# Kernel optimization log

Hardware: AMD Instinct MI355X
Metric: run time of the kernel (lower is better)

## Reference

```python
import jax, jax.numpy as jnp
import numpy as np

E, R, D, B = 1_000_000, 1_000, 64, 32_768
MARGIN = 1.0


def setup_inputs() -> dict:
    key = jax.random.key(0)
    ks = jax.random.split(key, 8)
    return {
        "ent_embeddings": jax.random.normal(ks[0], (E, D), dtype=jnp.float32) * (1.0 / np.sqrt(D)),
        "rel_matrices": jax.random.normal(ks[1], (R, D * D), dtype=jnp.float32) * (1.0 / D),
        "ph": jax.random.randint(ks[2], (B,), 0, E, dtype=jnp.int32),
        "pt": jax.random.randint(ks[3], (B,), 0, E, dtype=jnp.int32),
        "pr": jax.random.randint(ks[4], (B,), 0, R, dtype=jnp.int32),
        "nh": jax.random.randint(ks[5], (B,), 0, E, dtype=jnp.int32),
        "nt": jax.random.randint(ks[6], (B,), 0, E, dtype=jnp.int32),
        "nr": jax.random.randint(ks[7], (B,), 0, R, dtype=jnp.int32),
    }


def _score(ent, rel, h_idx, t_idx, r_idx):
    # gather: h,t -> [B,D]; r -> [B,D,D]
    h = ent[h_idx]
    t = ent[t_idx]
    r = rel[r_idx].reshape(-1, D, D)
    rt = jnp.einsum('bij,bj->bi', r, t)      # matmul(pr, pt): [B,D]
    # mean over D (keep_dims=False) then sum keepdims -> [B,1]
    return jnp.mean(h * rt, axis=1, keepdims=True)


def reference(ent_embeddings, rel_matrices, ph, pt, pr, nh, nt, nr):
    sp = _score(ent_embeddings, rel_matrices, ph, pt, pr)  # [B,1]
    sn = _score(ent_embeddings, rel_matrices, nh, nt, nr)  # [B,1]
    return jnp.sum(jnp.maximum(0.0, sn - sp + MARGIN))
```

## Files before the change

### kernel.cpp

```cpp
#include <hip/hip_runtime.h>


#define DIM 64
#define BATCH 32768
#define NREL 1000
#define NTASK (2 * BATCH)
#define BINCAP 128
#define RS 68
#define TS 36
#define SENT 0x7F800001u


__global__ __launch_bounds__(256) void scatter_kernel(
    const int* __restrict__ ph, const int* __restrict__ pt,
    const int* __restrict__ pr, const int* __restrict__ nh,
    const int* __restrict__ nt, const int* __restrict__ nr,
    int* __restrict__ cursors, int4* __restrict__ bins,
    unsigned int* __restrict__ pairs, float* __restrict__ out)
{
    int t = blockIdx.x * 256 + threadIdx.x;
    int b = t & (BATCH - 1);
    int side = t >> 15;
    int r  = side ? nr[b] : pr[b];
    int ti = side ? nt[b] : pt[b];
    int hi = side ? nh[b] : ph[b];
    int c = atomicAdd(&cursors[r], 1);
    if (c < BINCAP) bins[r * BINCAP + c] = make_int4(t, ti, hi, 0);
    pairs[b] = SENT;
    if (t == 0) *out = 0.f;
}

__global__ __launch_bounds__(256) void score_kernel(
    const float* __restrict__ ent, const float* __restrict__ rel,
    const int* __restrict__ cursors, const int4* __restrict__ bins,
    unsigned int* __restrict__ pairs, float* __restrict__ out)
{
    const int r = blockIdx.x;
    const int w = threadIdx.x >> 6;
    const int lane = threadIdx.x & 63;

    __shared__ float RT[DIM * RS];
    __shared__ float TT[4 * DIM * TS];
    float* bsum = &RT[64];
    if (threadIdx.x == 0) *bsum = 0.f;

    const float4* rg = (const float4*)(rel + (size_t)r * (DIM * DIM));
    #pragma unroll
    for (int it = 0; it < 4; ++it) {
        int f = threadIdx.x + 256 * it;
        int i = f >> 4, jc = f & 15;
        float4 v = rg[f];
        RT[(4 * jc + 0) * RS + i] = v.x;
        RT[(4 * jc + 1) * RS + i] = v.y;
        RT[(4 * jc + 2) * RS + i] = v.z;
        RT[(4 * jc + 3) * RS + i] = v.w;
    }

    const int start = r * BINCAP;
    const int cnt = min(cursors[r], BINCAP);
    const int tb = start + w * 32;
    const int nv = min(32, cnt - w * 32);

    float* tt = &TT[w * (DIM * TS)];
    if (nv > 0) {
        int m = lane & 31;
        int ch = lane >> 5;
        int4 e = bins[tb + min(m, nv - 1)];
        const float4* tr = (const float4*)(ent + (size_t)e.y * DIM);
        #pragma unroll
        for (int c = 0; c < 8; ++c) {
            float4 v = tr[ch * 8 + c];
            int j = ch * 32 + c * 4;
            tt[(j + 0) * TS + m] = v.x;
            tt[(j + 1) * TS + m] = v.y;
            tt[(j + 2) * TS + m] = v.z;
            tt[(j + 3) * TS + m] = v.w;
        }
    }
    __syncthreads();

    if (nv > 0) {
        const int mg = lane >> 3;
        const int ig = lane & 7;

        float4 h0v[4], h1v[4]; int tk[4];
        #pragma unroll
        for (int a = 0; a < 4; ++a) {
            int4 e = bins[tb + min(mg * 4 + a, nv - 1)];
            tk[a] = e.x;
            const float4* hr = (const float4*)(ent + (size_t)e.z * DIM);
            h0v[a] = hr[ig * 2];
            h1v[a] = hr[ig * 2 + 1];
        }

        float acc[4][8];
        #pragma unroll
        for (int a = 0; a < 4; ++a)
            #pragma unroll
            for (int b = 0; b < 8; ++b) acc[a][b] = 0.f;

        const float* ttA = tt + mg * 4;
        const float* rtB = RT + ig * 8;
        #pragma unroll 2
        for (int j = 0; j < 64; ++j) {
            float4 Av = *(const float4*)(ttA + j * TS);
            float4 B0 = *(const float4*)(rtB + j * RS);
            float4 B1 = *(const float4*)(rtB + j * RS + 4);
            float A_[4] = {Av.x, Av.y, Av.z, Av.w};
            float B_[8] = {B0.x, B0.y, B0.z, B0.w, B1.x, B1.y, B1.z, B1.w};
            #pragma unroll
            for (int a = 0; a < 4; ++a)
                #pragma unroll
                for (int b = 0; b < 8; ++b)
                    acc[a][b] = fmaf(A_[a], B_[b], acc[a][b]);
        }

        float wsum = 0.f;
        #pragma unroll
        for (int a = 0; a < 4; ++a) {
            float p = h0v[a].x * acc[a][0] + h0v[a].y * acc[a][1] +
                      h0v[a].z * acc[a][2] + h0v[a].w * acc[a][3] +
                      h1v[a].x * acc[a][4] + h1v[a].y * acc[a][5] +
                      h1v[a].z * acc[a][6] + h1v[a].w * acc[a][7];
            p += __shfl_xor(p, 1, 64);
            p += __shfl_xor(p, 2, 64);
            p += __shfl_xor(p, 4, 64);
            if (ig == 0 && mg * 4 + a < nv) {
                float s = p * (1.0f / DIM);
                int b = tk[a] & (BATCH - 1);
                int side = tk[a] >> 15;
                unsigned int old = atomicExch(&pairs[b], __float_as_uint(s));
                if (old != SENT) {
                    float o = __uint_as_float(old);
                    float sn = side ? s : o;
                    float sp = side ? o : s;
                    wsum += fmaxf(0.f, sn - sp + 1.0f);
                }
            }
        }
        #pragma unroll
        for (int off = 1; off < 64; off <<= 1)
            wsum += __shfl_xor(wsum, off, 64);
        if (lane == 0 && wsum != 0.f) atomicAdd(bsum, wsum);
    }

    __syncthreads();
    if (threadIdx.x == 0 && *bsum != 0.f) atomicAdd(out, *bsum);
}

extern "C" void kernel_launch(void* const* d_in, const int* in_sizes, int n_in,
                              void* d_out, int out_size, void* d_ws, size_t ws_size,
                              hipStream_t stream) {
    const float* ent = (const float*)d_in[0];
    const float* rel = (const float*)d_in[1];
    const int* ph = (const int*)d_in[2];
    const int* pt = (const int*)d_in[3];
    const int* pr = (const int*)d_in[4];
    const int* nh = (const int*)d_in[5];
    const int* nt = (const int*)d_in[6];
    const int* nr = (const int*)d_in[7];
    float* out = (float*)d_out;

    char* ws = (char*)d_ws;
    int* cursors         = (int*)(ws + 0);
    int4* bins           = (int4*)(ws + 4096);
    unsigned int* pairs  = (unsigned int*)(ws + 2052096);

    hipMemsetAsync(cursors, 0, 4096, stream);
    scatter_kernel<<<NTASK / 256, 256, 0, stream>>>(ph, pt, pr, nh, nt, nr,
                                                    cursors, bins, pairs, out);
    score_kernel<<<NREL, 256, 0, stream>>>(ent, rel, cursors, bins, pairs, out);
}
```

Measured before the change: 340.3 us.

## Process two relations per block, prefetching second tail gather during first tile

Measured after the change: 339.1 us, median of 2. About the same (-0.3%).

```diff
diff --git a/kernel.cpp b/kernel.cpp
--- a/kernel.cpp
+++ b/kernel.cpp
@@ -30,24 +30,12 @@
     if (t == 0) *out = 0.f;
 }
 
-__global__ __launch_bounds__(256) void score_kernel(
-    const float* __restrict__ ent, const float* __restrict__ rel,
-    const int* __restrict__ cursors, const int4* __restrict__ bins,
-    unsigned int* __restrict__ pairs, float* __restrict__ out)
-{
-    const int r = blockIdx.x;
-    const int w = threadIdx.x >> 6;
-    const int lane = threadIdx.x & 63;
-
-    __shared__ float RT[DIM * RS];
-    __shared__ float TT[4 * DIM * TS];
-    float* bsum = &RT[64];
-    if (threadIdx.x == 0) *bsum = 0.f;
-
-    const float4* rg = (const float4*)(rel + (size_t)r * (DIM * DIM));
+__device__ __forceinline__ void stage_RT(float* RT, const float* relrow, int tid)
+{
+    const float4* rg = (const float4*)relrow;
     #pragma unroll
     for (int it = 0; it < 4; ++it) {
-        int f = threadIdx.x + 256 * it;
+        int f = tid + 256 * it;
         int i = f >> 4, jc = f & 15;
         float4 v = rg[f];
         RT[(4 * jc + 0) * RS + i] = v.x;
@@ -55,95 +43,148 @@
         RT[(4 * jc + 2) * RS + i] = v.z;
         RT[(4 * jc + 3) * RS + i] = v.w;
     }
-
-    const int start = r * BINCAP;
-    const int cnt = min(cursors[r], BINCAP);
-    const int tb = start + w * 32;
-    const int nv = min(32, cnt - w * 32);
-
-    float* tt = &TT[w * (DIM * TS)];
-    if (nv > 0) {
-        int m = lane & 31;
-        int ch = lane >> 5;
-        int4 e = bins[tb + min(m, nv - 1)];
-        const float4* tr = (const float4*)(ent + (size_t)e.y * DIM);
-        #pragma unroll
-        for (int c = 0; c < 8; ++c) {
-            float4 v = tr[ch * 8 + c];
-            int j = ch * 32 + c * 4;
-            tt[(j + 0) * TS + m] = v.x;
-            tt[(j + 1) * TS + m] = v.y;
-            tt[(j + 2) * TS + m] = v.z;
-            tt[(j + 3) * TS + m] = v.w;
-        }
-    }
-    __syncthreads();
-
-    if (nv > 0) {
-        const int mg = lane >> 3;
-        const int ig = lane & 7;
-
-        float4 h0v[4], h1v[4]; int tk[4];
-        #pragma unroll
-        for (int a = 0; a < 4; ++a) {
-            int4 e = bins[tb + min(mg * 4 + a, nv - 1)];
-            tk[a] = e.x;
-            const float4* hr = (const float4*)(ent + (size_t)e.z * DIM);
-            h0v[a] = hr[ig * 2];
-            h1v[a] = hr[ig * 2 + 1];
-        }
-
-        float acc[4][8];
+}
+
+__device__ __forceinline__ void write_TT(float* tt, const float4* tv,
+                                         int m, int ch)
+{
+    #pragma unroll
+    for (int c = 0; c < 8; ++c) {
+        float4 v = tv[c];
+        int j = ch * 32 + c * 4;
+        tt[(j + 0) * TS + m] = v.x;
+        tt[(j + 1) * TS + m] = v.y;
+        tt[(j + 2) * TS + m] = v.z;
+        tt[(j + 3) * TS + m] = v.w;
+    }
+}
+
+__device__ __forceinline__ float do_tile(
+    const float* __restrict__ tt, const float* __restrict__ RT,
+    const float* __restrict__ ent, const int4* __restrict__ bins,
+    unsigned int* __restrict__ pairs, int tb, int nv, int mg, int ig)
+{
+    float4 h0v[4], h1v[4]; int tk[4];
+    #pragma unroll
+    for (int a = 0; a < 4; ++a) {
+        int4 e = bins[tb + min(mg * 4 + a, nv - 1)];
+        tk[a] = e.x;
+        const float4* hr = (const float4*)(ent + (size_t)e.z * DIM);
+        h0v[a] = hr[ig * 2];
+        h1v[a] = hr[ig * 2 + 1];
+    }
+
+    float acc[4][8];
+    #pragma unroll
+    for (int a = 0; a < 4; ++a)
+        #pragma unroll
+        for (int b = 0; b < 8; ++b) acc[a][b] = 0.f;
+
+    const float* ttA = tt + mg * 4;
+    const float* rtB = RT + ig * 8;
+    #pragma unroll 2
+    for (int j = 0; j < 64; ++j) {
+        float4 Av = *(const float4*)(ttA + j * TS);
+        float4 B0 = *(const float4*)(rtB + j * RS);
+        float4 B1 = *(const float4*)(rtB + j * RS + 4);
+        float A_[4] = {Av.x, Av.y, Av.z, Av.w};
+        float B_[8] = {B0.x, B0.y, B0.z, B0.w, B1.x, B1.y, B1.z, B1.w};
         #pragma unroll
         for (int a = 0; a < 4; ++a)
             #pragma unroll
-            for (int b = 0; b < 8; ++b) acc[a][b] = 0.f;
-
-        const float* ttA = tt + mg * 4;
-        const float* rtB = RT + ig * 8;
-        #pragma unroll 2
-        for (int j = 0; j < 64; ++j) {
-            float4 Av = *(const float4*)(ttA + j * TS);
-            float4 B0 = *(const float4*)(rtB + j * RS);
-            float4 B1 = *(const float4*)(rtB + j * RS + 4);
-            float A_[4] = {Av.x, Av.y, Av.z, Av.w};
-            float B_[8] = {B0.x, B0.y, B0.z, B0.w, B1.x, B1.y, B1.z, B1.w};
-            #pragma unroll
-            for (int a = 0; a < 4; ++a)
-                #pragma unroll
-                for (int b = 0; b < 8; ++b)
-                    acc[a][b] = fmaf(A_[a], B_[b], acc[a][b]);
-        }
-
-        float wsum = 0.f;
-        #pragma unroll
-        for (int a = 0; a < 4; ++a) {
-            float p = h0v[a].x * acc[a][0] + h0v[a].y * acc[a][1] +
-                      h0v[a].z * acc[a][2] + h0v[a].w * acc[a][3] +
-                      h1v[a].x * acc[a][4] + h1v[a].y * acc[a][5] +
-                      h1v[a].z * acc[a][6] + h1v[a].w * acc[a][7];
-            p += __shfl_xor(p, 1, 64);
-            p += __shfl_xor(p, 2, 64);
-            p += __shfl_xor(p, 4, 64);
-            if (ig == 0 && mg * 4 + a < nv) {
-                float s = p * (1.0f / DIM);
-                int b = tk[a] & (BATCH - 1);
-                int side = tk[a] >> 15;
-                unsigned int old = atomicExch(&pairs[b], __float_as_uint(s));
-                if (old != SENT) {
-                    float o = __uint_as_float(old);
-                    float sn = side ? s : o;
-                    float sp = side ? o : s;
-                    wsum += fmaxf(0.f, sn - sp + 1.0f);
-                }
+            for (int b = 0; b < 8; ++b)
+                acc[a][b] = fmaf(A_[a], B_[b], acc[a][b]);
+    }
+
+    float wsum = 0.f;
+    #pragma unroll
+    for (int a = 0; a < 4; ++a) {
+        float p = h0v[a].x * acc[a][0] + h0v[a].y * acc[a][1] +
+                  h0v[a].z * acc[a][2] + h0v[a].w * acc[a][3] +
+                  h1v[a].x * acc[a][4] + h1v[a].y * acc[a][5] +
+                  h1v[a].z * acc[a][6] + h1v[a].w * acc[a][7];
+        p += __shfl_xor(p, 1, 64);
+        p += __shfl_xor(p, 2, 64);
+        p += __shfl_xor(p, 4, 64);
+        if (ig == 0 && mg * 4 + a < nv) {
+            float s = p * (1.0f / DIM);
+            int b = tk[a] & (BATCH - 1);
+            int side = tk[a] >> 15;
+            unsigned int old = atomicExch(&pairs[b], __float_as_uint(s));
+            if (old != SENT) {
+                float o = __uint_as_float(old);
+                float sn = side ? s : o;
+                float sp = side ? o : s;
+                wsum += fmaxf(0.f, sn - sp + 1.0f);
             }
         }
-        #pragma unroll
-        for (int off = 1; off < 64; off <<= 1)
-            wsum += __shfl_xor(wsum, off, 64);
-        if (lane == 0 && wsum != 0.f) atomicAdd(bsum, wsum);
-    }
-
+    }
+    return wsum;
+}
+
+__global__ __launch_bounds__(256) void score_kernel(
+    const float* __restrict__ ent, const float* __restrict__ rel,
+    const int* __restrict__ cursors, const int4* __restrict__ bins,
+    unsigned int* __restrict__ pairs, float* __restrict__ out)
+{
+    const int r0 = blockIdx.x * 2;
+    const int r1 = r0 + 1;
+    const int w = threadIdx.x >> 6;
+    const int lane = threadIdx.x & 63;
+    const int m  = lane & 31;
+    const int ch = lane >> 5;
+    const int mg = lane >> 3;
+    const int ig = lane & 7;
+
+    __shared__ float RT[DIM * RS];
+    __shared__ float TT[4 * DIM * TS];
+    float* bsum = &RT[64];
+    if (threadIdx.x == 0) *bsum = 0.f;
+
+    const int cnt0 = min(cursors[r0], BINCAP);
+    const int cnt1 = min(cursors[r1], BINCAP);
+    const int tb0 = r0 * BINCAP + w * 32;
+    const int tb1 = r1 * BINCAP + w * 32;
+    const int nv0 = min(32, cnt0 - w * 32);
+    const int nv1 = min(32, cnt1 - w * 32);
+
+    float* tt = &TT[w * (DIM * TS)];
+
+    int4 e1;
+    if (nv0 > 0) {
+        int4 e0 = bins[tb0 + min(m, nv0 - 1)];
+        const float4* tr = (const float4*)(ent + (size_t)e0.y * DIM);
+        float4 tv[8];
+        #pragma unroll
+        for (int c = 0; c < 8; ++c) tv[c] = tr[ch * 8 + c];
+        write_TT(tt, tv, m, ch);
+    }
+    stage_RT(RT, rel + (size_t)r0 * (DIM * DIM), threadIdx.x);
+    if (nv1 > 0) e1 = bins[tb1 + min(m, nv1 - 1)];
+    __syncthreads();
+
+    float4 tv1[8];
+    if (nv1 > 0) {
+        const float4* tr = (const float4*)(ent + (size_t)e1.y * DIM);
+        #pragma unroll
+        for (int c = 0; c < 8; ++c) tv1[c] = tr[ch * 8 + c];
+    }
+    float wsum = 0.f;
+    if (nv0 > 0)
+        wsum += do_tile(tt, RT, ent, bins, pairs, tb0, nv0, mg, ig);
+    __syncthreads();
+
+    if (nv1 > 0) write_TT(tt, tv1, m, ch);
+    stage_RT(RT, rel + (size_t)r1 * (DIM * DIM), threadIdx.x);
+    __syncthreads();
+
+    if (nv1 > 0)
+        wsum += do_tile(tt, RT, ent, bins, pairs, tb1, nv1, mg, ig);
+
+    #pragma unroll
+    for (int off = 1; off < 64; off <<= 1)
+        wsum += __shfl_xor(wsum, off, 64);
+    if (lane == 0 && wsum != 0.f) atomicAdd(bsum, wsum);
     __syncthreads();
     if (threadIdx.x == 0 && *bsum != 0.f) atomicAdd(out, *bsum);
 }
@@ -169,5 +210,6 @@
     hipMemsetAsync(cursors, 0, 4096, stream);
     scatter_kernel<<<NTASK / 256, 256, 0, stream>>>(ph, pt, pr, nh, nt, nr,
                                                     cursors, bins, pairs, out);
-    score_kernel<<<NREL, 256, 0, stream>>>(ent, rel, cursors, bins, pairs, out);
-}
+    score_kernel<<<NREL / 2, 256, 0, stream>>>(ent, rel, cursors, bins,
+                                               pairs, out);
+}
```

## Compute per-relation R·t products with bf16 MFMA instead of fp32 FMAs

Applied to the files above, without the earlier changes.

After: 348.8 us. 1.02x slower.

```diff
diff --git a/kernel.cpp b/kernel.cpp
--- a/kernel.cpp
+++ b/kernel.cpp
@@ -6,10 +6,20 @@
 #define NREL 1000
 #define NTASK (2 * BATCH)
 #define BINCAP 128
-#define RS 68
-#define TS 36
+#define SRS 72
 #define SENT 0x7F800001u
 
+typedef __attribute__((ext_vector_type(8))) short bf16x8;
+typedef __attribute__((ext_vector_type(4))) float f32x4;
+
+
+__device__ __forceinline__ unsigned f2bf1(float x) {
+    unsigned u = __float_as_uint(x);
+    return (u + 0x7FFFu + ((u >> 16) & 1u)) >> 16;
+}
+__device__ __forceinline__ unsigned pack2(float a, float b) {
+    return f2bf1(a) | (f2bf1(b) << 16);
+}
 
 __global__ __launch_bounds__(256) void scatter_kernel(
     const int* __restrict__ ph, const int* __restrict__ pt,
@@ -38,11 +48,13 @@
     const int r = blockIdx.x;
     const int w = threadIdx.x >> 6;
     const int lane = threadIdx.x & 63;
+    const int row  = lane & 15;
+    const int quad = lane >> 4;
 
-    __shared__ float RT[DIM * RS];
-    __shared__ float TT[4 * DIM * TS];
-    float* bsum = &RT[64];
-    if (threadIdx.x == 0) *bsum = 0.f;
+    __shared__ __align__(16) unsigned short RR[DIM * SRS];
+    __shared__ __align__(16) unsigned short TT[4][32 * SRS];
+    __shared__ float bsum;
+    if (threadIdx.x == 0) bsum = 0.f;
 
     const float4* rg = (const float4*)(rel + (size_t)r * (DIM * DIM));
     #pragma unroll
@@ -50,18 +62,15 @@
         int f = threadIdx.x + 256 * it;
         int i = f >> 4, jc = f & 15;
         float4 v = rg[f];
-        RT[(4 * jc + 0) * RS + i] = v.x;
-        RT[(4 * jc + 1) * RS + i] = v.y;
-        RT[(4 * jc + 2) * RS + i] = v.z;
-        RT[(4 * jc + 3) * RS + i] = v.w;
+        unsigned* dst = (unsigned*)&RR[i * SRS + jc * 4];
+        dst[0] = pack2(v.x, v.y);
+        dst[1] = pack2(v.z, v.w);
     }
 
-    const int start = r * BINCAP;
     const int cnt = min(cursors[r], BINCAP);
-    const int tb = start + w * 32;
+    const int tb = r * BINCAP + w * 32;
     const int nv = min(32, cnt - w * 32);
 
-    float* tt = &TT[w * (DIM * TS)];
     if (nv > 0) {
         int m = lane & 31;
         int ch = lane >> 5;
@@ -70,82 +79,81 @@
         #pragma unroll
         for (int c = 0; c < 8; ++c) {
             float4 v = tr[ch * 8 + c];
-            int j = ch * 32 + c * 4;
-            tt[(j + 0) * TS + m] = v.x;
-            tt[(j + 1) * TS + m] = v.y;
-            tt[(j + 2) * TS + m] = v.z;
-            tt[(j + 3) * TS + m] = v.w;
+            unsigned* dst = (unsigned*)&TT[w][m * SRS + ch * 32 + c * 4];
+            dst[0] = pack2(v.x, v.y);
+            dst[1] = pack2(v.z, v.w);
         }
     }
     __syncthreads();
 
+    float wsum = 0.f;
     if (nv > 0) {
-        const int mg = lane >> 3;
-        const int ig = lane & 7;
+        f32x4 acc[2][4];
+        #pragma unroll
+        for (int mb = 0; mb < 2; ++mb)
+            #pragma unroll
+            for (int ib = 0; ib < 4; ++ib) {
+                f32x4 z = {0.f, 0.f, 0.f, 0.f};
+                acc[mb][ib] = z;
+            }
 
-        float4 h0v[4], h1v[4]; int tk[4];
+        const unsigned short* ttw = TT[w];
         #pragma unroll
-        for (int a = 0; a < 4; ++a) {
-            int4 e = bins[tb + min(mg * 4 + a, nv - 1)];
-            tk[a] = e.x;
-            const float4* hr = (const float4*)(ent + (size_t)e.z * DIM);
-            h0v[a] = hr[ig * 2];
-            h1v[a] = hr[ig * 2 + 1];
+        for (int kb = 0; kb < 2; ++kb) {
+            bf16x8 afr[2], bfr[4];
+            #pragma unroll
+            for (int mb = 0; mb < 2; ++mb)
+                afr[mb] = *(const bf16x8*)&ttw[(mb * 16 + row) * SRS +
+                                               kb * 32 + quad * 8];
+            #pragma unroll
+            for (int ib = 0; ib < 4; ++ib)
+                bfr[ib] = *(const bf16x8*)&RR[(ib * 16 + row) * SRS +
+                                              kb * 32 + quad * 8];
+            #pragma unroll
+            for (int mb = 0; mb < 2; ++mb)
+                #pragma unroll
+                for (int ib = 0; ib < 4; ++ib)
+                    acc[mb][ib] = __builtin_amdgcn_mfma_f32_16x16x32_bf16(
+                        afr[mb], bfr[ib], acc[mb][ib], 0, 0, 0);
         }
 
-        float acc[4][8];
         #pragma unroll
-        for (int a = 0; a < 4; ++a)
+        for (int mb = 0; mb < 2; ++mb) {
             #pragma unroll
-            for (int b = 0; b < 8; ++b) acc[a][b] = 0.f;
-
-        const float* ttA = tt + mg * 4;
-        const float* rtB = RT + ig * 8;
-        #pragma unroll 2
-        for (int j = 0; j < 64; ++j) {
-            float4 Av = *(const float4*)(ttA + j * TS);
-            float4 B0 = *(const float4*)(rtB + j * RS);
-            float4 B1 = *(const float4*)(rtB + j * RS + 4);
-            float A_[4] = {Av.x, Av.y, Av.z, Av.w};
-            float B_[8] = {B0.x, B0.y, B0.z, B0.w, B1.x, B1.y, B1.z, B1.w};
-            #pragma unroll
-            for (int a = 0; a < 4; ++a)
-                #pragma unroll
-                for (int b = 0; b < 8; ++b)
-                    acc[a][b] = fmaf(A_[a], B_[b], acc[a][b]);
-        }
-
-        float wsum = 0.f;
-        #pragma unroll
-        for (int a = 0; a < 4; ++a) {
-            float p = h0v[a].x * acc[a][0] + h0v[a].y * acc[a][1] +
-                      h0v[a].z * acc[a][2] + h0v[a].w * acc[a][3] +
-                      h1v[a].x * acc[a][4] + h1v[a].y * acc[a][5] +
-                      h1v[a].z * acc[a][6] + h1v[a].w * acc[a][7];
-            p += __shfl_xor(p, 1, 64);
-            p += __shfl_xor(p, 2, 64);
-            p += __shfl_xor(p, 4, 64);
-            if (ig == 0 && mg * 4 + a < nv) {
-                float s = p * (1.0f / DIM);
-                int b = tk[a] & (BATCH - 1);
-                int side = tk[a] >> 15;
-                unsigned int old = atomicExch(&pairs[b], __float_as_uint(s));
-                if (old != SENT) {
-                    float o = __uint_as_float(old);
-                    float sn = side ? s : o;
-                    float sp = side ? o : s;
-                    wsum += fmaxf(0.f, sn - sp + 1.0f);
+            for (int rr = 0; rr < 4; ++rr) {
+                int mm = mb * 16 + quad * 4 + rr;
+                int4 e = bins[tb + min(mm, nv - 1)];
+                const float* hr = ent + (size_t)e.z * DIM;
+                float p = hr[row]      * acc[mb][0][rr]
+                        + hr[row + 16] * acc[mb][1][rr]
+                        + hr[row + 32] * acc[mb][2][rr]
+                        + hr[row + 48] * acc[mb][3][rr];
+                p += __shfl_xor(p, 1, 64);
+                p += __shfl_xor(p, 2, 64);
+                p += __shfl_xor(p, 4, 64);
+                p += __shfl_xor(p, 8, 64);
+                if (row == 0 && mm < nv) {
+                    float s = p * (1.0f / DIM);
+                    int b = e.x & (BATCH - 1);
+                    int side = e.x >> 15;
+                    unsigned old = atomicExch(&pairs[b], __float_as_uint(s));
+                    if (old != SENT) {
+                        float o = __uint_as_float(old);
+                        float sn = side ? s : o;
+                        float sp = side ? o : s;
+                        wsum += fmaxf(0.f, sn - sp + 1.0f);
+                    }
                 }
             }
         }
-        #pragma unroll
-        for (int off = 1; off < 64; off <<= 1)
-            wsum += __shfl_xor(wsum, off, 64);
-        if (lane == 0 && wsum != 0.f) atomicAdd(bsum, wsum);
     }
 
+    #pragma unroll
+    for (int off = 1; off < 64; off <<= 1)
+        wsum += __shfl_xor(wsum, off, 64);
+    if (lane == 0 && wsum != 0.f) atomicAdd(&bsum, wsum);
     __syncthreads();
-    if (threadIdx.x == 0 && *bsum != 0.f) atomicAdd(out, *bsum);
+    if (threadIdx.x == 0 && bsum != 0.f) atomicAdd(out, bsum);
 }
 
 extern "C" void kernel_launch(void* const* d_in, const int* in_sizes, int n_in,
@@ -169,5 +177,6 @@
     hipMemsetAsync(cursors, 0, 4096, stream);
     scatter_kernel<<<NTASK / 256, 256, 0, stream>>>(ph, pt, pr, nh, nt, nr,
                                                     cursors, bins, pairs, out);
-    score_kernel<<<NREL, 256, 0, stream>>>(ent, rel, cursors, bins, pairs, out);
+    score_kernel<<<NREL, 256, 0, stream>>>(ent, rel, cursors, bins,
+                                           pairs, out);
 }
```
